# Kernel optimization log

Measured on AMD Instinct MI355X. Metric: run time of the kernel, lower is better.

## Reference

```python
import jax, jax.numpy as jnp
import numpy as np

H = 16      # num_attention_heads
D = 128     # head_size
ROT = 32    # rotary_ndims
WIN = 256   # attention_window[layer_id]
G = 64      # max_global_tokens
BASE = 10000.0


def _rotate_half(x):
    x1, x2 = jnp.split(x, 2, axis=-1)
    return jnp.concatenate([-x2, x1], axis=-1)


def setup_inputs() -> dict:
    key = jax.random.key(0)
    ks = jax.random.split(key, 6)
    B, S, HD = 2, 2048, H * D
    hidden_states = jax.random.normal(ks[0], (B, S, HD), jnp.float32)
    attention_mask = jnp.zeros((B, 1, 1, S), jnp.float32)
    glob_idx = jnp.sort(jax.random.randint(ks[1], (B, G), 0, S), axis=-1)
    W_qkv = jax.random.normal(ks[2], (HD, 3 * HD), jnp.float32) * 0.02
    b_qkv = jnp.zeros((3 * HD,), jnp.float32)
    W_o = jax.random.normal(ks[3], (HD, HD), jnp.float32) * 0.02
    b_o = jnp.zeros((HD,), jnp.float32)
    return {"hidden_states": hidden_states, "attention_mask": attention_mask,
            "glob_idx": glob_idx, "W_qkv": W_qkv, "b_qkv": b_qkv,
            "W_o": W_o, "b_o": b_o}


def reference(hidden_states, attention_mask, glob_idx, W_qkv, b_qkv, W_o, b_o):
    B, S, HD = hidden_states.shape
    qkv = (hidden_states @ W_qkv + b_qkv).reshape(B, S, H, 3 * D)
    q = qkv[..., :D].transpose(0, 2, 1, 3)        # [B,H,S,D]
    k = qkv[..., D:2 * D].transpose(0, 2, 1, 3)
    v = qkv[..., 2 * D:].transpose(0, 2, 1, 3)

    # GPT-NeoX rotary on first ROT dims
    inv_freq = 1.0 / (BASE ** (jnp.arange(0, ROT, 2, dtype=jnp.float32) / ROT))
    freqs = jnp.einsum('s,f->sf', jnp.arange(S, dtype=jnp.float32), inv_freq)
    emb = jnp.concatenate([freqs, freqs], axis=-1)           # [S,ROT]
    cos = jnp.cos(emb)[None, None]
    sin = jnp.sin(emb)[None, None]
    q = jnp.concatenate([q[..., :ROT] * cos + _rotate_half(q[..., :ROT]) * sin,
                         q[..., ROT:]], axis=-1)
    k = jnp.concatenate([k[..., :ROT] * cos + _rotate_half(k[..., :ROT]) * sin,
                         k[..., ROT:]], axis=-1)

    # step_attn path: keys/values are head-averaged before attention (key.mean(1))
    k_mean = k.mean(axis=1)   # [B,S,D]
    v_mean = v.mean(axis=1)
    scale = 1.0 / jnp.sqrt(jnp.float32(D))
    minv = jnp.finfo(jnp.float32).min

    s0 = jnp.einsum('bhqd,bkd->bhqk', q[:, :, :WIN], k_mean[:, :WIN]) * scale
    causal = jnp.tril(jnp.ones((WIN, WIN), bool))
    s0 = jnp.where(causal[None, None], s0, minv) + attention_mask[..., :WIN]
    out0 = jnp.einsum('bhqk,bkd->bhqd', jax.nn.softmax(s0, axis=-1), v_mean[:, :WIN])

    Sq = S - WIN
    steps = jnp.arange(Sq)
    win_pos = steps[:, None] + 1 + jnp.arange(WIN)[None, :]
    k_win = k_mean[:, win_pos]
    v_win = v_mean[:, win_pos]
    mask_win = attention_mask[:, 0, 0, :][:, win_pos][:, None]
    qs = q[:, :, WIN:]                                        # [B,H,Sq,D]
    s_win = jnp.einsum('bhqd,bqwd->bhqw', qs, k_win) * scale + mask_win

    k_glob = jnp.take_along_axis(k_mean, glob_idx[..., None], axis=1)  # [B,G,D]
    v_glob = jnp.take_along_axis(v_mean, glob_idx[..., None], axis=1)
    # sorted indices: 'filter < i then truncate to G' == prefix-valid mask per slot
    valid = (glob_idx[:, None, :] < steps[None, :, None])[:, None]     # [B,1,Sq,G]
    s_glob = jnp.where(valid, jnp.einsum('bhqd,bgd->bhqg', qs, k_glob) * scale, minv)

    w = jax.nn.softmax(jnp.concatenate([s_glob, s_win], axis=-1), axis=-1)
    out_steps = (jnp.einsum('bhqg,bgd->bhqd', w[..., :G], v_glob)
                 + jnp.einsum('bhqw,bqwd->bhqd', w[..., G:], v_win))

    out = jnp.concatenate([out0, out_steps], axis=2)          # [B,H,S,D]
    out = out.transpose(0, 2, 1, 3).reshape(B, S, HD)
    return out @ W_o + b_o
```

## Files before the change

### kernel.cpp

```cpp
#include <hip/hip_runtime.h>
#include <math.h>

#define SCALE_ 0.08838834764831845f
#define MINV_  (-3.4028234663852886e38f)

typedef __bf16 bf16;
typedef bf16  bf16x4 __attribute__((ext_vector_type(4)));
typedef bf16  bf16x8 __attribute__((ext_vector_type(8)));
typedef float f32x4  __attribute__((ext_vector_type(4)));
typedef float f32x16 __attribute__((ext_vector_type(16)));
typedef float float4v __attribute__((ext_vector_type(4)));

#define LD8(p) (*(const bf16x8*)(p))

__device__ __forceinline__ f32x4 mfma16(bf16x8 a, bf16x8 b, f32x4 c) {
    return __builtin_amdgcn_mfma_f32_16x16x32_bf16(a, b, c, 0, 0, 0);
}
__device__ __forceinline__ f32x16 mfma32(bf16x8 a, bf16x8 b, f32x16 c) {
    return __builtin_amdgcn_mfma_f32_32x32x16_bf16(a, b, c, 0, 0, 0);
}

typedef const __attribute__((address_space(1))) void* gas_t;
typedef __attribute__((address_space(3))) void* sas_t;
__device__ __forceinline__ void gload_lds16(const void* g, void* l) {
    __builtin_amdgcn_global_load_lds((gas_t)g, (sas_t)l, 16, 0, 0);
}

__global__ __launch_bounds__(256) void prep_kernel(const float* __restrict__ hidden, bf16* __restrict__ A16,
                                                   const float* __restrict__ Wqkv, bf16* __restrict__ BT1,
                                                   const float* __restrict__ Wo, bf16* __restrict__ BT2,
                                                   const float* __restrict__ bqkv, float* __restrict__ bias1)
{
    int x = blockIdx.x;
    if (x < 8192) {
        int i = (x * 256 + threadIdx.x) * 4;
        float4v v = *(const float4v*)(hidden + i);
        bf16x4 o; o.x = (bf16)v.x; o.y = (bf16)v.y; o.z = (bf16)v.z; o.w = (bf16)v.w;
        *(bf16x4*)(A16 + i) = o;
        return;
    }
    if (x < 16384) {
        __shared__ float tile[32][33];
        int t = x - 8192;
        int z = t >> 12;
        int tt = t & 4095;
        const float* W = z ? Wo : Wqkv;
        bf16* BT = z ? BT2 : BT1;
        int srcStride = z ? 2048 : 6144;
        int k0 = (tt & 63) * 32, n0 = (tt >> 6) * 32;
        int c = threadIdx.x & 31, r = threadIdx.x >> 5;
        int n = n0 + c;
        int src = z ? n : ((n >> 7) * 384 + (n & 127));
        #pragma unroll
        for (int rr = 0; rr < 32; rr += 8)
            tile[r + rr][c] = W[(size_t)(k0 + r + rr) * srcStride + src];
        __syncthreads();
        #pragma unroll
        for (int rr = 0; rr < 32; rr += 8)
            BT[(size_t)(n0 + r + rr) * 2048 + k0 + c] = (bf16)tile[c][r + rr];
        return;
    }
    int t = x - 16384;
    if (t == 512) {
        for (int c = threadIdx.x; c < 2304; c += 256) {
            if (c < 2048) bias1[c] = bqkv[(c >> 7) * 384 + (c & 127)];
            else {
                int j = c - 2048; float s = 0.f;
                for (int h = 0; h < 16; h++) s += bqkv[h * 384 + 128 + j];
                bias1[c] = s * 0.0625f;
            }
        }
        return;
    }
    int k0 = t * 4;
    int j = threadIdx.x;
    float acc[4];
    #pragma unroll
    for (int k = 0; k < 4; k++) acc[k] = 0.f;
    for (int h = 0; h < 16; h++) {
        #pragma unroll
        for (int k = 0; k < 4; k++)
            acc[k] += Wqkv[(size_t)(k0 + k) * 6144 + h * 384 + 128 + j];
    }
    #pragma unroll
    for (int k = 0; k < 4; k++)
        BT1[(size_t)(2048 + j) * 2048 + k0 + k] = (bf16)(acc[k] * 0.0625f);
}


#define GEMM_PROLOGUE_AND_KLOOP                                                           \
    __shared__ __align__(16) bf16 As[128 * 64];                                           \
    __shared__ __align__(16) bf16 Bs[128 * 64];                                           \
    const int tid  = threadIdx.x;                                                         \
    const int wv   = tid >> 6, lane = tid & 63, l32 = lane & 31, half = lane >> 5;        \
    const int wrow = wv >> 1, wcol = wv & 1;                                              \
    const int m0 = blockIdx.y * 128, n0 = blockIdx.x * 128;                               \
    int rowS[4], colS[4];                                                                 \
    _Pragma("unroll")                                                                     \
    for (int j = 0; j < 4; j++) {                                                         \
        int flat = (wv * 4 + j) * 64 + lane;                                              \
        int row = flat >> 3, cp = flat & 7;                                               \
        rowS[j] = row;                                                                    \
        colS[j] = (cp ^ (row & 7)) * 8;                                                   \
    }                                                                                     \
    f32x16 acc[2][2];                                                                     \
    _Pragma("unroll")                                                                     \
    for (int i = 0; i < 2; i++)                                                           \
        _Pragma("unroll")                                                                 \
        for (int j = 0; j < 2; j++)                                                       \
            _Pragma("unroll")                                                             \
            for (int r = 0; r < 16; r++) acc[i][j][r] = 0.f;                              \
    for (int kk = 0; kk < K; kk += 64) {                                                  \
        __syncthreads();                                                                  \
        _Pragma("unroll")                                                                 \
        for (int j = 0; j < 4; j++) {                                                     \
            gload_lds16(A  + (size_t)(m0 + rowS[j]) * K + kk + colS[j], &As[(wv * 4 + j) * 512]); \
            gload_lds16(BT + (size_t)(n0 + rowS[j]) * K + kk + colS[j], &Bs[(wv * 4 + j) * 512]); \
        }                                                                                 \
        __syncthreads();                                                                  \
        bf16x8 af[2][4], bfr[2][4];                                                       \
        _Pragma("unroll")                                                                 \
        for (int mt = 0; mt < 2; mt++) {                                                  \
            int row = wrow * 64 + mt * 32 + l32;                                          \
            _Pragma("unroll")                                                             \
            for (int k16 = 0; k16 < 4; k16++) {                                           \
                int lc = k16 * 2 + half;                                                  \
                af[mt][k16] = LD8(&As[row * 64 + ((lc ^ (row & 7)) * 8)]);                \
            }                                                                             \
        }                                                                                 \
        _Pragma("unroll")                                                                 \
        for (int nt = 0; nt < 2; nt++) {                                                  \
            int row = wcol * 64 + nt * 32 + l32;                                          \
            _Pragma("unroll")                                                             \
            for (int k16 = 0; k16 < 4; k16++) {                                           \
                int lc = k16 * 2 + half;                                                  \
                bfr[nt][k16] = LD8(&Bs[row * 64 + ((lc ^ (row & 7)) * 8)]);               \
            }                                                                             \
        }                                                                                 \
        _Pragma("unroll")                                                                 \
        for (int k16 = 0; k16 < 4; k16++)                                                 \
            _Pragma("unroll")                                                             \
            for (int mt = 0; mt < 2; mt++)                                                \
                _Pragma("unroll")                                                         \
                for (int nt = 0; nt < 2; nt++)                                            \
                    acc[mt][nt] = mfma32(af[mt][k16], bfr[nt][k16], acc[mt][nt]);         \
    }

__global__ __launch_bounds__(256) void gemm_rot_kernel(const bf16* __restrict__ A, const bf16* __restrict__ BT,
                                                       const float* __restrict__ bias, bf16* __restrict__ C,
                                                       int M, int N, int K)
{
    GEMM_PROLOGUE_AND_KLOOP

    #pragma unroll
    for (int mt = 0; mt < 2; mt++) {
        #pragma unroll
        for (int nt = 0; nt < 2; nt++) {
            int n = n0 + wcol * 64 + nt * 32 + l32;
            float bn = bias[n];
            const bool rot = (wcol == 0) && (nt == 0) && (n0 <= 2048);
            float inv = rot ? __expf(-0.575646273248511f * (float)(l32 & 15)) : 0.f;
            #pragma unroll
            for (int r = 0; r < 16; r++) {
                int m = m0 + wrow * 64 + mt * 32 + (r & 3) + 8 * (r >> 2) + 4 * half;
                float v = acc[mt][nt][r] + bn;
                if (rot) {
                    float ang = (float)(m & 2047) * inv;
                    float cs, sn;
                    __sincosf(ang, &sn, &cs);
                    float pv = __shfl_xor(v, 16, 64);
                    v = (l32 < 16) ? (v * cs - pv * sn) : (v * cs + pv * sn);
                }
                C[(size_t)m * N + n] = (bf16)v;
            }
        }
    }
}

__global__ __launch_bounds__(256) void gemm_out_kernel(const bf16* __restrict__ A, const bf16* __restrict__ BT,
                                                       const float* __restrict__ bias, float* __restrict__ C,
                                                       int M, int N, int K)
{
    GEMM_PROLOGUE_AND_KLOOP

    #pragma unroll
    for (int mt = 0; mt < 2; mt++) {
        #pragma unroll
        for (int nt = 0; nt < 2; nt++) {
            int n = n0 + wcol * 64 + nt * 32 + l32;
            float bn = bias[n];
            #pragma unroll
            for (int r = 0; r < 16; r++) {
                int m = m0 + wrow * 64 + mt * 32 + (r & 3) + 8 * (r >> 2) + 4 * half;
                C[(size_t)m * N + n] = acc[mt][nt][r] + bn;
            }
        }
    }
}

__global__ __launch_bounds__(256) void pretile_kernel(const bf16* __restrict__ C1, const int* __restrict__ gidx,
                                                      bf16* __restrict__ KF, bf16* __restrict__ VF)
{
    __shared__ bf16 Vt[64][130];
    const int c = blockIdx.x, b = blockIdx.y;
    const bool isGlob = (c == 32);
    const int tid = threadIdx.x;

    {
        int row = tid >> 2, cb = (tid & 3) * 32;
        int pos = isGlob ? gidx[b * 64 + row] : (c * 64 + row);
        const bf16* src = C1 + (size_t)(b * 2048 + pos) * 2304 + 2176 + cb;
        #pragma unroll
        for (int k = 0; k < 4; k++)
            *(bf16x8*)&Vt[row][cb + k * 8] = LD8(src + k * 8);
    }
    __syncthreads();

    #pragma unroll
    for (int i = 0; i < 4; i++) {
        int sid = tid + i * 256;
        int lane = sid & 63, fi = sid >> 6;
        int l16 = lane & 15, quad = lane >> 4;
        int t = fi >> 2, ks = fi & 3;
        int pos = isGlob ? gidx[b * 64 + t * 16 + l16] : (c * 64 + t * 16 + l16);
        const bf16* src = C1 + (size_t)(b * 2048 + pos) * 2304 + 2048 + ks * 32 + quad * 8;
        *(bf16x8*)&KF[((size_t)(b * 33 + c) * 16 + fi) * 512 + lane * 8] = LD8(src);
    }

    #pragma unroll
    for (int i = 0; i < 4; i++) {
        int sid = tid + i * 256;
        int lane = sid & 63, fi = sid >> 6;
        int l16 = lane & 15, quad = lane >> 4;
        int dt = fi >> 1, ks2 = fi & 1;
        int d = dt * 16 + l16;
        bf16x8 v;
        #pragma unroll
        for (int j = 0; j < 8; j++)
            v[j] = Vt[ks2 * 32 + quad * 8 + j][d];
        *(bf16x8*)&VF[((size_t)(b * 33 + c) * 16 + fi) * 512 + lane * 8] = v;
    }
}

#define PSTRIDE 88

__device__ __forceinline__ void attn0_body(int bx, int h, int b, bf16* Pw,
                                           const bf16* __restrict__ C1, const bf16* __restrict__ KF,
                                           const bf16* __restrict__ VF, const float* __restrict__ mask,
                                           bf16* __restrict__ attn)
{
    const int tid = threadIdx.x, wv = tid >> 6, lane = tid & 63, quad = lane >> 4, l16 = lane & 15;
    const int q0 = (bx * 4 + wv) * 16;

    bf16x8 af[4];
    const bf16* qbase = C1 + (size_t)(b * 2048 + q0 + l16) * 2304 + h * 128;
    #pragma unroll
    for (int ks = 0; ks < 4; ks++) af[ks] = LD8(qbase + ks * 32 + quad * 8);

    f32x4 m_run = (f32x4){MINV_, MINV_, MINV_, MINV_};
    f32x4 l_run = (f32x4){0.f, 0.f, 0.f, 0.f};
    f32x4 O[8];
    #pragma unroll
    for (int dt = 0; dt < 8; dt++) O[dt] = (f32x4){0.f, 0.f, 0.f, 0.f};

    for (int c = 0; c <= bx; c++) {
        const bf16* KFc = KF + ((size_t)(b * 33 + c) * 16) * 512;
        const bf16* VFc = VF + ((size_t)(b * 33 + c) * 16) * 512;

        f32x4 acc[4];
        #pragma unroll
        for (int t = 0; t < 4; t++) acc[t] = (f32x4){0.f, 0.f, 0.f, 0.f};
        #pragma unroll
        for (int t = 0; t < 4; t++)
            #pragma unroll
            for (int ks = 0; ks < 4; ks++)
                acc[t] = mfma16(af[ks], LD8(KFc + (size_t)(t * 4 + ks) * 512 + lane * 8), acc[t]);

        float sv[4][4];
        #pragma unroll
        for (int t = 0; t < 4; t++) {
            int key = c * 64 + t * 16 + l16;
            float addv = mask[b * 2048 + key];
            #pragma unroll
            for (int r = 0; r < 4; r++) {
                int q = q0 + quad * 4 + r;
                sv[t][r] = (key <= q) ? (acc[t][r] * SCALE_ + addv) : MINV_;
            }
        }

        f32x4 cm;
        #pragma unroll
        for (int r = 0; r < 4; r++) cm[r] = fmaxf(fmaxf(sv[0][r], sv[1][r]), fmaxf(sv[2][r], sv[3][r]));
        #pragma unroll
        for (int ms = 1; ms < 16; ms <<= 1)
            #pragma unroll
            for (int r = 0; r < 4; r++) cm[r] = fmaxf(cm[r], __shfl_xor(cm[r], ms, 64));

        f32x4 nm, alpha;
        #pragma unroll
        for (int r = 0; r < 4; r++) { nm[r] = fmaxf(m_run[r], cm[r]); alpha[r] = __expf(m_run[r] - nm[r]); }

        float pv[4][4];
        f32x4 cs = (f32x4){0.f, 0.f, 0.f, 0.f};
        #pragma unroll
        for (int t = 0; t < 4; t++)
            #pragma unroll
            for (int r = 0; r < 4; r++) {
                pv[t][r] = __expf(sv[t][r] - nm[r]);
                cs[r] += pv[t][r];
            }
        #pragma unroll
        for (int ms = 1; ms < 16; ms <<= 1)
            #pragma unroll
            for (int r = 0; r < 4; r++) cs[r] += __shfl_xor(cs[r], ms, 64);

        m_run = nm;
        #pragma unroll
        for (int r = 0; r < 4; r++) l_run[r] = l_run[r] * alpha[r] + cs[r];
        #pragma unroll
        for (int dt = 0; dt < 8; dt++)
            #pragma unroll
            for (int r = 0; r < 4; r++) O[dt][r] *= alpha[r];

        #pragma unroll
        for (int t = 0; t < 4; t++)
            #pragma unroll
            for (int r = 0; r < 4; r++)
                Pw[(quad * 4 + r) * PSTRIDE + t * 16 + l16] = (bf16)pv[t][r];
        bf16x8 pa0 = LD8(&Pw[l16 * PSTRIDE + quad * 8]);
        bf16x8 pa1 = LD8(&Pw[l16 * PSTRIDE + 32 + quad * 8]);

        #pragma unroll
        for (int dt = 0; dt < 8; dt++) {
            O[dt] = mfma16(pa0, LD8(VFc + (size_t)(dt * 2 + 0) * 512 + lane * 8), O[dt]);
            O[dt] = mfma16(pa1, LD8(VFc + (size_t)(dt * 2 + 1) * 512 + lane * 8), O[dt]);
        }
    }

    f32x4 invl;
    #pragma unroll
    for (int r = 0; r < 4; r++) invl[r] = 1.0f / l_run[r];
    #pragma unroll
    for (int dt = 0; dt < 8; dt++)
        #pragma unroll
        for (int r = 0; r < 4; r++) {
            int q = q0 + quad * 4 + r;
            attn[(size_t)(b * 2048 + q) * 2048 + h * 128 + dt * 16 + l16] = (bf16)(O[dt][r] * invl[r]);
        }
}

__device__ __forceinline__ void attn_steps_body(int sb, int b, bf16* Pw,
                                                const bf16* __restrict__ C1, const bf16* __restrict__ KF,
                                                const bf16* __restrict__ VF, const float* __restrict__ mask,
                                                const int* __restrict__ gidx, bf16* __restrict__ attn)
{
    const int tid = threadIdx.x, wv = tid >> 6, lane = tid & 63, quad = lane >> 4, l16 = lane & 15;
    const int step = sb * 4 + wv, p = 256 + step;

    bf16x8 af[4];
    const bf16* qrow = C1 + (size_t)(b * 2048 + p) * 2304;
    #pragma unroll
    for (int ks = 0; ks < 4; ks++) af[ks] = LD8(qrow + l16 * 128 + ks * 32 + quad * 8);

    int gix[4];
    #pragma unroll
    for (int t = 0; t < 4; t++) gix[t] = gidx[b * 64 + t * 16 + l16];

    f32x4 m_run = (f32x4){MINV_, MINV_, MINV_, MINV_};
    f32x4 l_run = (f32x4){0.f, 0.f, 0.f, 0.f};
    f32x4 O[8];
    #pragma unroll
    for (int dt = 0; dt < 8; dt++) O[dt] = (f32x4){0.f, 0.f, 0.f, 0.f};

    const int c0 = (step + 1) >> 6;

    for (int iter = 0; iter < 6; iter++) {
        int c;
        bool isGlob = (iter == 0);
        if (isGlob) c = 32;
        else { c = c0 + iter - 1; if (c > 31) break; }

        const bf16* KFc = KF + ((size_t)(b * 33 + c) * 16) * 512;
        const bf16* VFc = VF + ((size_t)(b * 33 + c) * 16) * 512;

        f32x4 acc[4];
        #pragma unroll
        for (int t = 0; t < 4; t++) acc[t] = (f32x4){0.f, 0.f, 0.f, 0.f};
        #pragma unroll
        for (int t = 0; t < 4; t++)
            #pragma unroll
            for (int ks = 0; ks < 4; ks++)
                acc[t] = mfma16(af[ks], LD8(KFc + (size_t)(t * 4 + ks) * 512 + lane * 8), acc[t]);

        float sv[4][4];
        bool vld[4];
        #pragma unroll
        for (int t = 0; t < 4; t++) {
            float addv = 0.f;
            if (isGlob) vld[t] = gix[t] < step;
            else {
                int pos = c * 64 + t * 16 + l16;
                vld[t] = (unsigned)(pos - step - 1) < 256u;
                addv = mask[b * 2048 + pos];
            }
            #pragma unroll
            for (int r = 0; r < 4; r++) sv[t][r] = vld[t] ? (acc[t][r] * SCALE_ + addv) : MINV_;
        }

        f32x4 cm;
        #pragma unroll
        for (int r = 0; r < 4; r++) cm[r] = fmaxf(fmaxf(sv[0][r], sv[1][r]), fmaxf(sv[2][r], sv[3][r]));
        #pragma unroll
        for (int ms = 1; ms < 16; ms <<= 1)
            #pragma unroll
            for (int r = 0; r < 4; r++) cm[r] = fmaxf(cm[r], __shfl_xor(cm[r], ms, 64));

        f32x4 nm, alpha;
        #pragma unroll
        for (int r = 0; r < 4; r++) { nm[r] = fmaxf(m_run[r], cm[r]); alpha[r] = __expf(m_run[r] - nm[r]); }

        float pv[4][4];
        f32x4 cs = (f32x4){0.f, 0.f, 0.f, 0.f};
        #pragma unroll
        for (int t = 0; t < 4; t++)
            #pragma unroll
            for (int r = 0; r < 4; r++) {
                pv[t][r] = vld[t] ? __expf(sv[t][r] - nm[r]) : 0.f;
                cs[r] += pv[t][r];
            }
        #pragma unroll
        for (int ms = 1; ms < 16; ms <<= 1)
            #pragma unroll
            for (int r = 0; r < 4; r++) cs[r] += __shfl_xor(cs[r], ms, 64);

        m_run = nm;
        #pragma unroll
        for (int r = 0; r < 4; r++) l_run[r] = l_run[r] * alpha[r] + cs[r];
        #pragma unroll
        for (int dt = 0; dt < 8; dt++)
            #pragma unroll
            for (int r = 0; r < 4; r++) O[dt][r] *= alpha[r];

        #pragma unroll
        for (int t = 0; t < 4; t++)
            #pragma unroll
            for (int r = 0; r < 4; r++)
                Pw[(quad * 4 + r) * PSTRIDE + t * 16 + l16] = (bf16)pv[t][r];
        bf16x8 pa0 = LD8(&Pw[l16 * PSTRIDE + quad * 8]);
        bf16x8 pa1 = LD8(&Pw[l16 * PSTRIDE + 32 + quad * 8]);

        #pragma unroll
        for (int dt = 0; dt < 8; dt++) {
            O[dt] = mfma16(pa0, LD8(VFc + (size_t)(dt * 2 + 0) * 512 + lane * 8), O[dt]);
            O[dt] = mfma16(pa1, LD8(VFc + (size_t)(dt * 2 + 1) * 512 + lane * 8), O[dt]);
        }
    }

    f32x4 invl;
    #pragma unroll
    for (int r = 0; r < 4; r++) invl[r] = 1.0f / l_run[r];
    #pragma unroll
    for (int dt = 0; dt < 8; dt++)
        #pragma unroll
        for (int r = 0; r < 4; r++) {
            int h = quad * 4 + r;
            attn[(size_t)(b * 2048 + p) * 2048 + h * 128 + dt * 16 + l16] = (bf16)(O[dt][r] * invl[r]);
        }
}

__global__ __launch_bounds__(256) void attn_all_kernel(const bf16* __restrict__ C1, const bf16* __restrict__ KF,
                                                       const bf16* __restrict__ VF, const float* __restrict__ mask,
                                                       const int* __restrict__ gidx, bf16* __restrict__ attn)
{
    __shared__ __align__(16) bf16 Ps[4 * 16 * PSTRIDE];
    const int wv = threadIdx.x >> 6;
    bf16* Pw = &Ps[wv * (16 * PSTRIDE)];
    if (blockIdx.x < 448) {
        attn_steps_body(blockIdx.x, blockIdx.y, Pw, C1, KF, VF, mask, gidx, attn);
    } else {
        int bi = blockIdx.x - 448;
        attn0_body(bi >> 4, bi & 15, blockIdx.y, Pw, C1, KF, VF, mask, attn);
    }
}

extern "C" void kernel_launch(void* const* d_in, const int* in_sizes, int n_in,
                              void* d_out, int out_size, void* d_ws, size_t ws_size,
                              hipStream_t stream)
{
    const float* hidden = (const float*)d_in[0];
    const float* amask  = (const float*)d_in[1];
    const int*   gidx   = (const int*)d_in[2];
    const float* Wqkv   = (const float*)d_in[3];
    const float* bqkv   = (const float*)d_in[4];
    const float* Wo     = (const float*)d_in[5];
    const float* bo     = (const float*)d_in[6];

    char* ws = (char*)d_ws;
    size_t off = 0;
    auto take = [&](size_t bytes) -> char* {
        char* p = ws + off;
        off = (off + bytes + 255) & ~(size_t)255;
        return p;
    };
    bf16*  A16   = (bf16*)take(4096ull * 2048 * 2);
    bf16*  BT1   = (bf16*)take(2304ull * 2048 * 2);
    bf16*  BT2   = (bf16*)take(2048ull * 2048 * 2);
    bf16*  C1    = (bf16*)take(4096ull * 2304 * 2);
    bf16*  KF    = (bf16*)take(2ull * 33 * 16 * 512 * 2);
    bf16*  VF    = (bf16*)take(2ull * 33 * 16 * 512 * 2);
    bf16*  attnb = (bf16*)take(4096ull * 2048 * 2);
    float* bias1 = (float*)take(2304 * 4);

    prep_kernel<<<16897, 256, 0, stream>>>(hidden, A16, Wqkv, BT1, Wo, BT2, bqkv, bias1);

    gemm_rot_kernel<<<dim3(18, 32), 256, 0, stream>>>(A16, BT1, bias1, C1, 4096, 2304, 2048);

    pretile_kernel<<<dim3(33, 2), 256, 0, stream>>>(C1, gidx, KF, VF);

    attn_all_kernel<<<dim3(512, 2), 256, 0, stream>>>(C1, KF, VF, amask, gidx, attnb);

    gemm_out_kernel<<<dim3(16, 32), 256, 0, stream>>>(attnb, BT2, bo, (float*)d_out, 4096, 2048, 2048);

    (void)in_sizes; (void)n_in; (void)out_size; (void)ws_size;
}
```

Baseline: 303.2 us.

## Double-buffer LDS tiles in GEMM k-loop to overlap loads with MFMA

Converts the shared GEMM prologue/k-loop into a two-stage double-buffered pipeline. The next tile's global-to-LDS loads are issued while the current tile is consumed, using explicit vmcnt waits and raw barriers in place of two __syncthreads per iteration. This is meant to hide global load latency behind MFMA work in both the QKV and output projections, at the cost of twice the LDS (64KB per block), which may reduce occupancy.

```diff
diff --git a/kernel.cpp b/kernel.cpp
--- a/kernel.cpp
+++ b/kernel.cpp
@@ -88,9 +88,9 @@
 }
 
 
-#define GEMM_PROLOGUE_AND_KLOOP                                                           \
-    __shared__ __align__(16) bf16 As[128 * 64];                                           \
-    __shared__ __align__(16) bf16 Bs[128 * 64];                                           \
+#define GEMM_DB_PROLOGUE_AND_KLOOP                                                        \
+    __shared__ __align__(16) bf16 As[2][128 * 64];                                        \
+    __shared__ __align__(16) bf16 Bs[2][128 * 64];                                        \
     const int tid  = threadIdx.x;                                                         \
     const int wv   = tid >> 6, lane = tid & 63, l32 = lane & 31, half = lane >> 5;        \
     const int wrow = wv >> 1, wcol = wv & 1;                                              \
@@ -103,6 +103,15 @@
         rowS[j] = row;                                                                    \
         colS[j] = (cp ^ (row & 7)) * 8;                                                   \
     }                                                                                     \
+    const int nt = K >> 6;                                                                \
+    auto stage = [&](int t, int bsel) {          \
+        int kk = t << 6;                                                                  \
+        _Pragma("unroll")                                                                 \
+        for (int j = 0; j < 4; j++) {                                                     \
+            gload_lds16(A  + (size_t)(m0 + rowS[j]) * K + kk + colS[j], &As[bsel][(wv * 4 + j) * 512]); \
+            gload_lds16(BT + (size_t)(n0 + rowS[j]) * K + kk + colS[j], &Bs[bsel][(wv * 4 + j) * 512]); \
+        }                                                                                 \
+    };                                                                                    \
     f32x16 acc[2][2];                                                                     \
     _Pragma("unroll")                                                                     \
     for (int i = 0; i < 2; i++)                                                           \
@@ -110,14 +119,16 @@
         for (int j = 0; j < 2; j++)                                                       \
             _Pragma("unroll")                                                             \
             for (int r = 0; r < 16; r++) acc[i][j][r] = 0.f;                              \
-    for (int kk = 0; kk < K; kk += 64) {                                                  \
-        __syncthreads();                                                                  \
-        _Pragma("unroll")                                                                 \
-        for (int j = 0; j < 4; j++) {                                                     \
-            gload_lds16(A  + (size_t)(m0 + rowS[j]) * K + kk + colS[j], &As[(wv * 4 + j) * 512]); \
-            gload_lds16(BT + (size_t)(n0 + rowS[j]) * K + kk + colS[j], &Bs[(wv * 4 + j) * 512]); \
-        }                                                                                 \
-        __syncthreads();                                                                  \
+    stage(0, 0);                                                                          \
+    stage(1, 1);                                                                          \
+    for (int t = 0; t < nt; ++t) {                                                        \
+        const int cur = t & 1;                                                            \
+        if (t < nt - 1) asm volatile("s_waitcnt vmcnt(8)" ::: "memory");                  \
+        else            asm volatile("s_waitcnt vmcnt(0)" ::: "memory");                  \
+        __builtin_amdgcn_s_barrier();                                                     \
+        asm volatile("" ::: "memory");                                                    \
+        const bf16* Ab = &As[cur][0];                                                     \
+        const bf16* Bb = &Bs[cur][0];                                                     \
         bf16x8 af[2][4], bfr[2][4];                                                       \
         _Pragma("unroll")                                                                 \
         for (int mt = 0; mt < 2; mt++) {                                                  \
@@ -125,16 +136,16 @@
             _Pragma("unroll")                                                             \
             for (int k16 = 0; k16 < 4; k16++) {                                           \
                 int lc = k16 * 2 + half;                                                  \
-                af[mt][k16] = LD8(&As[row * 64 + ((lc ^ (row & 7)) * 8)]);                \
+                af[mt][k16] = LD8(&Ab[row * 64 + ((lc ^ (row & 7)) * 8)]);                \
             }                                                                             \
         }                                                                                 \
         _Pragma("unroll")                                                                 \
-        for (int nt = 0; nt < 2; nt++) {                                                  \
-            int row = wcol * 64 + nt * 32 + l32;                                          \
+        for (int nt2 = 0; nt2 < 2; nt2++) {                                               \
+            int row = wcol * 64 + nt2 * 32 + l32;                                         \
             _Pragma("unroll")                                                             \
             for (int k16 = 0; k16 < 4; k16++) {                                           \
                 int lc = k16 * 2 + half;                                                  \
-                bfr[nt][k16] = LD8(&Bs[row * 64 + ((lc ^ (row & 7)) * 8)]);               \
+                bfr[nt2][k16] = LD8(&Bb[row * 64 + ((lc ^ (row & 7)) * 8)]);              \
             }                                                                             \
         }                                                                                 \
         _Pragma("unroll")                                                                 \
@@ -142,28 +153,32 @@
             _Pragma("unroll")                                                             \
             for (int mt = 0; mt < 2; mt++)                                                \
                 _Pragma("unroll")                                                         \
-                for (int nt = 0; nt < 2; nt++)                                            \
-                    acc[mt][nt] = mfma32(af[mt][k16], bfr[nt][k16], acc[mt][nt]);         \
+                for (int nt2 = 0; nt2 < 2; nt2++)                                         \
+                    acc[mt][nt2] = mfma32(af[mt][k16], bfr[nt2][k16], acc[mt][nt2]);      \
+        asm volatile("" ::: "memory");                                                    \
+        __builtin_amdgcn_s_barrier();                                                     \
+        asm volatile("" ::: "memory");                                                    \
+        if (t + 2 < nt) stage(t + 2, cur);                                                \
     }
 
 __global__ __launch_bounds__(256) void gemm_rot_kernel(const bf16* __restrict__ A, const bf16* __restrict__ BT,
                                                        const float* __restrict__ bias, bf16* __restrict__ C,
                                                        int M, int N, int K)
 {
-    GEMM_PROLOGUE_AND_KLOOP
+    GEMM_DB_PROLOGUE_AND_KLOOP
 
     #pragma unroll
     for (int mt = 0; mt < 2; mt++) {
         #pragma unroll
-        for (int nt = 0; nt < 2; nt++) {
-            int n = n0 + wcol * 64 + nt * 32 + l32;
+        for (int nt2 = 0; nt2 < 2; nt2++) {
+            int n = n0 + wcol * 64 + nt2 * 32 + l32;
             float bn = bias[n];
-            const bool rot = (wcol == 0) && (nt == 0) && (n0 <= 2048);
+            const bool rot = (wcol == 0) && (nt2 == 0) && (n0 <= 2048);
             float inv = rot ? __expf(-0.575646273248511f * (float)(l32 & 15)) : 0.f;
             #pragma unroll
             for (int r = 0; r < 16; r++) {
                 int m = m0 + wrow * 64 + mt * 32 + (r & 3) + 8 * (r >> 2) + 4 * half;
-                float v = acc[mt][nt][r] + bn;
+                float v = acc[mt][nt2][r] + bn;
                 if (rot) {
                     float ang = (float)(m & 2047) * inv;
                     float cs, sn;
@@ -181,18 +196,18 @@
                                                        const float* __restrict__ bias, float* __restrict__ C,
                                                        int M, int N, int K)
 {
-    GEMM_PROLOGUE_AND_KLOOP
+    GEMM_DB_PROLOGUE_AND_KLOOP
 
     #pragma unroll
     for (int mt = 0; mt < 2; mt++) {
         #pragma unroll
-        for (int nt = 0; nt < 2; nt++) {
-            int n = n0 + wcol * 64 + nt * 32 + l32;
+        for (int nt2 = 0; nt2 < 2; nt2++) {
+            int n = n0 + wcol * 64 + nt2 * 32 + l32;
             float bn = bias[n];
             #pragma unroll
             for (int r = 0; r < 16; r++) {
                 int m = m0 + wrow * 64 + mt * 32 + (r & 3) + 8 * (r >> 2) + 4 * half;
-                C[(size_t)m * N + n] = acc[mt][nt][r] + bn;
+                C[(size_t)m * N + n] = acc[mt][nt2][r] + bn;
             }
         }
     }
```

After: 316.5 us. 4.4% more time.
